# Optimization experiments

Hardware: AMD Instinct MI355X
Metric: run time of the kernel (lower is better)

Reference implementation:

```python
import jax, jax.numpy as jnp
import numpy as np

N, S, D, H = 2048, 16, 128, 8
EPS = 1e-5  # torch.nn.LayerNorm default eps


def setup_inputs() -> dict:
    key = jax.random.key(0)
    ks = jax.random.split(key, 3)
    return {
        "x": jax.random.normal(ks[0], (N, S, D), jnp.float32),
        "Wi": jax.random.normal(ks[1], (H, S, D, D), jnp.float32),
        "Wj": jax.random.normal(ks[2], (H, S, 2 * D, D), jnp.float32),
        "ln1_w": jnp.ones((S, D), jnp.float32),
        "ln1_b": jnp.zeros((S, D), jnp.float32),
        "prelu1_a": jnp.float32(0.25),  # torch PReLU default single param
        "ln2_w": jnp.ones((H, D), jnp.float32),
        "ln2_b": jnp.zeros((H, D), jnp.float32),
        "prelu2_a": jnp.float32(0.25),
    }


def _layernorm2(x, w, b):
    # LayerNorm over the last two dims (matches torch LayerNorm([A, B]))
    mu = jnp.mean(x, axis=(-2, -1), keepdims=True)
    var = jnp.var(x, axis=(-2, -1), keepdims=True)
    return (x - mu) * jax.lax.rsqrt(var + EPS) * w + b


def _prelu(x, a):
    return jnp.where(x >= 0, x, a * x)


def reference(x, Wi, Wj, ln1_w, ln1_b, prelu1_a, ln2_w, ln2_b, prelu2_a):
    n, s, d = x.shape
    h = Wi.shape[0]
    # sort descending along source dim
    idx = jnp.argsort(-x, axis=1)                      # [N,S,D] int
    x_sort = jnp.take_along_axis(x, idx, axis=1)       # [N,S,D]
    # pad with a zero row, take adjacent differences
    pad = jnp.concatenate([x_sort, jnp.zeros((n, 1, d), x.dtype)], axis=1)
    diff = pad[:, :-1, :] - pad[:, 1:, :]              # [N,S,D]
    # positional encoding: cumsum of 2^rank / 2^S
    enc = jnp.cumsum(jnp.exp2(idx.astype(x.dtype)), axis=1) / jnp.asarray(2.0 ** s, x.dtype)
    # per-head, per-source batched matmul with Wi
    se = jnp.einsum('bsd,hsdo->bhso', enc, Wi)         # [N,H,S,D]
    se = _prelu(_layernorm2(se, ln1_w, ln1_b), prelu1_a)  # Dropout in eval mode = identity
    cat = jnp.concatenate(
        [jnp.broadcast_to(diff[:, None, :, :], (n, h, s, d)), se], axis=-1
    )                                                  # [N,H,S,2D]
    out = jnp.einsum('bhsd,hsdo->bho', cat, Wj)        # [N,H,D]
    return _prelu(_layernorm2(out, ln2_w, ln2_b), prelu2_a)
```

## Files before the change

### kernel.cpp

```cpp
#include <hip/hip_runtime.h>

#define N_ 2048
#define S_ 16
#define D_ 128
#define H_ 8
#define EPS_ 1e-5f

typedef unsigned short ushortT;
typedef unsigned int uint32;
typedef __attribute__((ext_vector_type(8))) short short8;
typedef __attribute__((ext_vector_type(8))) unsigned short ushort8;
typedef __attribute__((ext_vector_type(4))) float f32x4;
typedef __attribute__((ext_vector_type(4))) unsigned int uint4v;
typedef __attribute__((ext_vector_type(8))) float float8;

__device__ __forceinline__ ushortT f2bf(float f) {
  union { float f; uint32 u; } c; c.f = f;
  uint32 u = c.u;
  u = (u + 0x7FFFu + ((u >> 16) & 1u)) >> 16;
  return (ushortT)u;
}
__device__ __forceinline__ float bf2f(ushortT b) {
  union { uint32 u; float f; } c; c.u = ((uint32)b) << 16;
  return c.f;
}

__global__ __launch_bounds__(256) void k_prep(const float* __restrict__ x,
                                              ushortT* __restrict__ enc,
                                              ushortT* __restrict__ diff) {
  int g = blockIdx.x * 256 + threadIdx.x;
  int n = g >> 7, d = g & 127;
  const float* xp = x + (size_t)n * (S_ * D_) + d;
  float v[S_];
#pragma unroll
  for (int s = 0; s < S_; ++s) v[s] = xp[s * D_];
  int r[S_];
#pragma unroll
  for (int i = 0; i < S_; ++i) {
    int ri = 0;
#pragma unroll
    for (int j = 0; j < S_; ++j)
      ri += ((v[j] > v[i]) || (v[j] == v[i] && j < i)) ? 1 : 0;
    r[i] = ri;
  }
  float xs[S_ + 1];
#pragma unroll
  for (int s = 0; s < S_; ++s) {
    float acc = 0.f;
#pragma unroll
    for (int i = 0; i < S_; ++i) acc += (r[i] == s) ? v[i] : 0.f;
    xs[s] = acc;
  }
  xs[S_] = 0.f;
  ushortT* ep = enc + (size_t)n * (S_ * D_) + d;
  ushortT* dp = diff + (size_t)n * (S_ * D_) + d;
#pragma unroll
  for (int s = 0; s < S_; ++s) {
    uint32 mm = 0;
#pragma unroll
    for (int i = 0; i < S_; ++i) mm |= (r[i] <= s) ? (1u << i) : 0u;
    ep[s * D_] = f2bf((float)mm * (1.f / 65536.f));
    dp[s * D_] = f2bf(xs[s] - xs[s + 1]);
  }
}

__global__ __launch_bounds__(256) void k_castW(const float* __restrict__ Wi,
                                               const float* __restrict__ Wj,
                                               ushortT* __restrict__ Wit,
                                               ushortT* __restrict__ Wjt) {
  __shared__ ushortT tile[128 * 136];
  int bx = blockIdx.x;
  int t = threadIdx.x;
  if (bx < 128) {
    int hs = bx;
    const float* src = Wi + (size_t)hs * D_ * D_;
#pragma unroll 4
    for (int i = 0; i < 64; ++i) {
      int e = t + 256 * i;
      int dd = e >> 7, o = e & 127;
      tile[dd * 136 + o] = f2bf(src[e]);
    }
    __syncthreads();
    int o = t >> 1, dbase = (t & 1) * 64;
    ushortT* dst = Wit + ((size_t)hs * D_ + o) * D_ + dbase;
#pragma unroll
    for (int c = 0; c < 8; ++c) {
      uint4v pk;
#pragma unroll
      for (int q = 0; q < 4; ++q) {
        ushortT lo = tile[(dbase + c * 8 + q * 2) * 136 + o];
        ushortT hi = tile[(dbase + c * 8 + q * 2 + 1) * 136 + o];
        pk[q] = (uint32)lo | ((uint32)hi << 16);
      }
      *(uint4v*)(dst + c * 8) = pk;
    }
  } else {
    int hs = bx - 128; int h = hs >> 4, s = hs & 15;
    const float* src = Wj + (size_t)hs * 256 * D_;
    for (int half = 0; half < 2; ++half) {
      if (half) __syncthreads();
#pragma unroll 4
      for (int i = 0; i < 64; ++i) {
        int e = t + 256 * i;
        int dd = e >> 7, o = e & 127;
        tile[dd * 136 + o] = f2bf(src[half * 16384 + e]);
      }
      __syncthreads();
      int o = t >> 1, db = (t & 1) * 64;
      ushortT* dst = Wjt + ((size_t)(h * D_ + o)) * (S_ * 256) + s * 256 + half * 128 + db;
#pragma unroll
      for (int c = 0; c < 8; ++c) {
        uint4v pk;
#pragma unroll
        for (int q = 0; q < 4; ++q) {
          ushortT lo = tile[(db + c * 8 + q * 2) * 136 + o];
          ushortT hi = tile[(db + c * 8 + q * 2 + 1) * 136 + o];
          pk[q] = (uint32)lo | ((uint32)hi << 16);
        }
        *(uint4v*)(dst + c * 8) = pk;
      }
    }
  }
}

__global__ __launch_bounds__(256) void k_gemm1(const ushortT* __restrict__ enc,
                                               const ushortT* __restrict__ Wit,
                                               ushortT* __restrict__ se,
                                               float* __restrict__ ssum,
                                               float* __restrict__ ssq) {
  int bt = blockIdx.x, s = blockIdx.y, hp = blockIdx.z;
  int h0 = hp * 4;
  __shared__ ushortT As[128 * 128];
  __shared__ ushortT Bs[128 * 128];
  int tid = threadIdx.x;
  int c16 = tid & 15, prow = tid >> 4;
  int wave = tid >> 6, lane = tid & 63;
  int l15 = lane & 15, lg = lane >> 4;

  ushort8 rb[8];
#pragma unroll
  for (int i = 0; i < 8; ++i) {
    int row = prow + 16 * i;
    int sw = ((c16 ^ (row & 7)) * 8);
    ushort8 va = *(const ushort8*)(enc + (size_t)(bt * 128 + row) * (S_ * D_) + s * D_ + c16 * 8);
    *(ushort8*)(As + row * 128 + sw) = va;
    rb[i] = *(const ushort8*)(Wit + ((size_t)((h0 * S_ + s) * D_) + row) * D_ + c16 * 8);
  }
  __syncthreads();
  short8 afr[4][2];
#pragma unroll
  for (int kk = 0; kk < 4; ++kk)
#pragma unroll
    for (int i = 0; i < 2; ++i) {
      int row = wave * 32 + i * 16 + l15;
      int cc = kk * 4 + lg;
      afr[kk][i] = *(const short8*)(As + row * 128 + ((cc ^ (row & 7)) * 8));
    }

  for (int hh = 0; hh < 4; ++hh) {
    int h = h0 + hh;
    if (hh) __syncthreads();
#pragma unroll
    for (int i = 0; i < 8; ++i) {
      int row = prow + 16 * i;
      *(ushort8*)(Bs + row * 128 + ((c16 ^ (row & 7)) * 8)) = rb[i];
    }
    if (hh < 3) {
#pragma unroll
      for (int i = 0; i < 8; ++i) {
        int row = prow + 16 * i;
        rb[i] = *(const ushort8*)(Wit + ((size_t)(((h + 1) * S_ + s) * D_) + row) * D_ + c16 * 8);
      }
    }
    __syncthreads();
    f32x4 acc[2][8];
#pragma unroll
    for (int i = 0; i < 2; ++i)
#pragma unroll
      for (int j = 0; j < 8; ++j) acc[i][j] = (f32x4)(0.f);
#pragma unroll
    for (int kk = 0; kk < 4; ++kk) {
      int cc = kk * 4 + lg;
      short8 b[8];
#pragma unroll
      for (int j = 0; j < 8; ++j) {
        int row = j * 16 + l15;
        b[j] = *(const short8*)(Bs + row * 128 + ((cc ^ (row & 7)) * 8));
      }
#pragma unroll
      for (int i = 0; i < 2; ++i)
#pragma unroll
        for (int j = 0; j < 8; ++j)
          acc[i][j] = __builtin_amdgcn_mfma_f32_16x16x32_bf16(afr[kk][i], b[j], acc[i][j], 0, 0, 0);
    }
#pragma unroll
    for (int i = 0; i < 2; ++i)
#pragma unroll
      for (int rr = 0; rr < 4; ++rr) {
        int rloc = wave * 32 + i * 16 + lg * 4 + rr;
        int b_g = bt * 128 + rloc;
        float rs = 0.f, rq = 0.f;
#pragma unroll
        for (int j = 0; j < 8; ++j) {
          float val = acc[i][j][rr];
          rs += val; rq += val * val;
        }
#pragma unroll
        for (int m = 1; m <= 8; m <<= 1) {
          rs += __shfl_xor(rs, m);
          rq += __shfl_xor(rq, m);
        }
        if (l15 == 0) {
          ssum[((size_t)s * N_ + b_g) * H_ + h] = rs;
          ssq[((size_t)s * N_ + b_g) * H_ + h] = rq;
        }
      }
    __syncthreads();
#pragma unroll
    for (int i = 0; i < 2; ++i)
#pragma unroll
      for (int rr = 0; rr < 4; ++rr) {
        int row = wave * 32 + i * 16 + lg * 4 + rr;
        int sw = (row & 7) << 3;
#pragma unroll
        for (int j = 0; j < 8; ++j) {
          int o = j * 16 + l15;
          Bs[row * 128 + (o ^ sw)] = f2bf(acc[i][j][rr]);
        }
      }
    __syncthreads();
#pragma unroll
    for (int p = 0; p < 2; ++p) {
      int row = p * 64 + (tid >> 2);
      int sw = (row & 7) << 3;
      int b_g = bt * 128 + row;
      ushortT* dst = se + (((size_t)b_g * H_ + h) * S_ + s) * D_;
#pragma unroll
      for (int q = 0; q < 4; ++q) {
        int o0 = (q * 4 + (tid & 3)) * 8;
        *(uint4v*)(dst + o0) = *(const uint4v*)(Bs + row * 128 + (o0 ^ sw));
      }
    }
  }
}

__global__ __launch_bounds__(256) void k_finalize(const float* __restrict__ ssum,
                                                  const float* __restrict__ ssq,
                                                  float* __restrict__ mr) {
  int t = blockIdx.x * 256 + threadIdx.x;
  float s1 = 0.f, s2 = 0.f;
#pragma unroll
  for (int s = 0; s < S_; ++s) {
    s1 += ssum[(size_t)s * (N_ * H_) + t];
    s2 += ssq[(size_t)s * (N_ * H_) + t];
  }
  float mu = s1 * (1.f / 2048.f);
  float var = s2 * (1.f / 2048.f) - mu * mu;
  mr[t * 2] = mu;
  mr[t * 2 + 1] = rsqrtf(var + EPS_);
}

__global__ __launch_bounds__(256, 3) void k_gemm2(const ushortT* __restrict__ diff,
                                                  const ushortT* __restrict__ se,
                                                  const ushortT* __restrict__ Wjt,
                                                  const float* __restrict__ mr,
                                                  const float* __restrict__ ln1w,
                                                  const float* __restrict__ ln1b,
                                                  const float* __restrict__ pa1,
                                                  float* __restrict__ outp,
                                                  int scount) {
  int bt = blockIdx.x, sh = blockIdx.y, h = blockIdx.z;
  int s0 = sh * scount;
  __shared__ ushortT As[128 * 64];
  __shared__ ushortT Bs[128 * 64];
  int tid = threadIdx.x;
  int c8 = tid & 7, trow = tid >> 3;
  int swst = ((c8 ^ (trow & 7)) * 8);
  int wave = tid >> 6, lane = tid & 63;
  int l15 = lane & 15, lg = lane >> 4;
  int wm = wave >> 1, wn = wave & 1;
  float a1 = pa1[0];

  float mu_r[4], rs_r[4];
  uint32 aoff_d[4], aoff_s[4], boff[4];
#pragma unroll
  for (int i = 0; i < 4; ++i) {
    int row = i * 32 + trow;
    int b_g = bt * 128 + row;
    mu_r[i] = mr[((size_t)b_g * H_ + h) * 2];
    rs_r[i] = mr[((size_t)b_g * H_ + h) * 2 + 1];
    aoff_d[i] = (uint32)b_g * (S_ * D_) + c8 * 8;
    aoff_s[i] = ((uint32)b_g * H_ + h) * (S_ * D_) + c8 * 8;
    boff[i] = (uint32)(h * D_ + row) * (S_ * 256) + c8 * 8;
  }
  ushort8 ra[4], rb[4];
  int nc = scount * 4;
  {
    uint32 add = s0 * D_;
#pragma unroll
    for (int i = 0; i < 4; ++i) {
      ra[i] = *(const ushort8*)(diff + aoff_d[i] + add);
      rb[i] = *(const ushort8*)(Wjt + boff[i] + s0 * 256);
    }
  }
  f32x4 acc[4][4];
#pragma unroll
  for (int i = 0; i < 4; ++i)
#pragma unroll
    for (int j = 0; j < 4; ++j) acc[i][j] = (f32x4)(0.f);

  for (int c = 0; c < nc; ++c) {
    int p = c & 3, s = s0 + (c >> 2);
    if (c) __syncthreads();
    if (p >= 2) {
      float8 w8 = *(const float8*)(ln1w + s * D_ + (p & 1) * 64 + c8 * 8);
      float8 b8 = *(const float8*)(ln1b + s * D_ + (p & 1) * 64 + c8 * 8);
#pragma unroll
      for (int i = 0; i < 4; ++i) {
        ushort8 v = ra[i];
#pragma unroll
        for (int e = 0; e < 8; ++e) {
          float f = bf2f(v[e]);
          float y = (f - mu_r[i]) * rs_r[i] * w8[e] + b8[e];
          y = (y >= 0.f) ? y : a1 * y;
          v[e] = f2bf(y);
        }
        ra[i] = v;
      }
    }
#pragma unroll
    for (int i = 0; i < 4; ++i) {
      int row = i * 32 + trow;
      *(ushort8*)(As + row * 64 + swst) = ra[i];
      *(ushort8*)(Bs + row * 64 + swst) = rb[i];
    }
    if (c + 1 < nc) {
      int cn = c + 1;
      int sn = s0 + (cn >> 2), pn = cn & 3;
      uint32 add = sn * D_ + (pn & 1) * 64;
      uint32 badd = sn * 256 + pn * 64;
#pragma unroll
      for (int i = 0; i < 4; ++i) {
        ra[i] = (pn < 2) ? *(const ushort8*)(diff + aoff_d[i] + add)
                         : *(const ushort8*)(se + aoff_s[i] + add);
        rb[i] = *(const ushort8*)(Wjt + boff[i] + badd);
      }
    }
    __syncthreads();
#pragma unroll
    for (int kk = 0; kk < 2; ++kk) {
      int cc = kk * 4 + lg;
      short8 a[4], b[4];
#pragma unroll
      for (int i = 0; i < 4; ++i) {
        int row = wm * 64 + i * 16 + l15;
        a[i] = *(const short8*)(As + row * 64 + ((cc ^ (row & 7)) * 8));
      }
#pragma unroll
      for (int j = 0; j < 4; ++j) {
        int row = wn * 64 + j * 16 + l15;
        b[j] = *(const short8*)(Bs + row * 64 + ((cc ^ (row & 7)) * 8));
      }
#pragma unroll
      for (int i = 0; i < 4; ++i)
#pragma unroll
        for (int j = 0; j < 4; ++j)
          acc[i][j] = __builtin_amdgcn_mfma_f32_16x16x32_bf16(a[i], b[j], acc[i][j], 0, 0, 0);
    }
  }
#pragma unroll
  for (int i = 0; i < 4; ++i)
#pragma unroll
    for (int j = 0; j < 4; ++j)
#pragma unroll
      for (int rr = 0; rr < 4; ++rr) {
        int b_g = bt * 128 + wm * 64 + i * 16 + lg * 4 + rr;
        int o = wn * 64 + j * 16 + l15;
        outp[(((size_t)sh * N_ + b_g) * H_ + h) * D_ + o] = acc[i][j][rr];
      }
}

__global__ __launch_bounds__(256) void k_ln2(const float* __restrict__ outp,
                                             const float* __restrict__ ln2w,
                                             const float* __restrict__ ln2b,
                                             const float* __restrict__ pa2,
                                             float* __restrict__ out,
                                             int nsplit) {
  int b = blockIdx.x, t = threadIdx.x;
  __shared__ float red[8];
  __shared__ float stats[2];
  f32x4 v = (f32x4)(0.f);
  for (int p = 0; p < nsplit; ++p)
    v += *((const f32x4*)(outp + (size_t)p * (N_ * 1024) + (size_t)b * 1024) + t);
  float s1 = v[0] + v[1] + v[2] + v[3];
  float s2 = v[0] * v[0] + v[1] * v[1] + v[2] * v[2] + v[3] * v[3];
#pragma unroll
  for (int m = 1; m <= 32; m <<= 1) {
    s1 += __shfl_xor(s1, m);
    s2 += __shfl_xor(s2, m);
  }
  int wave = t >> 6, lane = t & 63;
  if (lane == 0) { red[wave] = s1; red[4 + wave] = s2; }
  __syncthreads();
  if (t == 0) {
    float S = red[0] + red[1] + red[2] + red[3];
    float Q = red[4] + red[5] + red[6] + red[7];
    float mu = S * (1.f / 1024.f);
    float var = Q * (1.f / 1024.f) - mu * mu;
    stats[0] = mu; stats[1] = rsqrtf(var + EPS_);
  }
  __syncthreads();
  float mu = stats[0], rstd = stats[1];
  float a2 = pa2[0];
  f32x4 wv = *((const f32x4*)ln2w + t);
  f32x4 bv = *((const f32x4*)ln2b + t);
  f32x4 r;
#pragma unroll
  for (int e = 0; e < 4; ++e) {
    float y = (v[e] - mu) * rstd * wv[e] + bv[e];
    r[e] = (y >= 0.f) ? y : a2 * y;
  }
  *((f32x4*)(out + (size_t)b * 1024) + t) = r;
}

extern "C" void kernel_launch(void* const* d_in, const int* in_sizes, int n_in,
                              void* d_out, int out_size, void* d_ws, size_t ws_size,
                              hipStream_t stream) {
  const float* x    = (const float*)d_in[0];
  const float* Wi   = (const float*)d_in[1];
  const float* Wj   = (const float*)d_in[2];
  const float* ln1w = (const float*)d_in[3];
  const float* ln1b = (const float*)d_in[4];
  const float* pa1  = (const float*)d_in[5];
  const float* ln2w = (const float*)d_in[6];
  const float* ln2b = (const float*)d_in[7];
  const float* pa2  = (const float*)d_in[8];
  char* ws = (char*)d_ws;
  ushortT* se   = (ushortT*)(ws + 0);
  ushortT* diff = (ushortT*)(ws + 67108864);
  ushortT* Wjt  = (ushortT*)(ws + 75497472);
  float*   outp = (float*)(ws + 83886080);
  ushortT* enc  = (ushortT*)(ws + 83886080);
  ushortT* Wit  = (ushortT*)(ws + 92274688);
  float*   ssum = (float*)(ws + 96468992);
  float*   ssq  = (float*)(ws + 97517568);
  float*   out  = (float*)d_out;

  int nsplit = (ws_size >= 117571584ull) ? 4 : 2;
  int scount = S_ / nsplit;
  float* mr = (float*)(ws + 83886080 + (size_t)nsplit * 8388608);

  hipLaunchKernelGGL(k_prep, dim3(1024), dim3(256), 0, stream, x, enc, diff);
  hipLaunchKernelGGL(k_castW, dim3(256), dim3(256), 0, stream, Wi, Wj, Wit, Wjt);
  hipLaunchKernelGGL(k_gemm1, dim3(16, 16, 2), dim3(256), 0, stream, enc, Wit, se, ssum, ssq);
  hipLaunchKernelGGL(k_finalize, dim3(64), dim3(256), 0, stream, ssum, ssq, mr);
  hipLaunchKernelGGL(k_gemm2, dim3(16, nsplit, 8), dim3(256), 0, stream, diff, se, Wjt, mr,
                     ln1w, ln1b, pa1, outp, scount);
  hipLaunchKernelGGL(k_ln2, dim3(2048), dim3(256), 0, stream, outp, ln2w, ln2b, pa2, out, nsplit);
}
```

Baseline: 208.1 us.

## Pre-swizzle gemm2 operands and stream them to LDS with double buffering

k_prep and k_castW now write diff and Wj in a tile-contiguous, pre-swizzled layout. k_gemm2 can then copy 128x64 tiles straight from global memory into LDS with global_load_lds, using double-buffered A/B tiles so loads overlap the MFMA work. The LayerNorm1+PReLU applied to the se half is folded into fused multiply-adds using a precomputed rstd and -mu*rstd, and it packs to bf16 with v_cvt_pk_bf16_f32. Occupancy drops from 3 to 2 blocks per CU because LDS use doubles, and the indexing in the producer kernels gets more involved.

```diff
diff --git a/kernel.cpp b/kernel.cpp
--- a/kernel.cpp
+++ b/kernel.cpp
@@ -27,7 +27,7 @@
 
 __global__ __launch_bounds__(256) void k_prep(const float* __restrict__ x,
                                               ushortT* __restrict__ enc,
-                                              ushortT* __restrict__ diff) {
+                                              ushortT* __restrict__ diff_sw) {
   int g = blockIdx.x * 256 + threadIdx.x;
   int n = g >> 7, d = g & 127;
   const float* xp = x + (size_t)n * (S_ * D_) + d;
@@ -53,21 +53,23 @@
   }
   xs[S_] = 0.f;
   ushortT* ep = enc + (size_t)n * (S_ * D_) + d;
-  ushortT* dp = diff + (size_t)n * (S_ * D_) + d;
+  int btq = n >> 7, rr = n & 127, pp = d >> 6, c8p = (d >> 3) & 7, ee = d & 7;
+  int q = rr * 8 + (c8p ^ (rr & 7));
 #pragma unroll
   for (int s = 0; s < S_; ++s) {
     uint32 mm = 0;
 #pragma unroll
     for (int i = 0; i < S_; ++i) mm |= (r[i] <= s) ? (1u << i) : 0u;
     ep[s * D_] = f2bf((float)mm * (1.f / 65536.f));
-    dp[s * D_] = f2bf(xs[s] - xs[s + 1]);
+    size_t idx = ((((size_t)(btq * 16 + s) * 2 + pp) * 1024) + q) * 8 + ee;
+    diff_sw[idx] = f2bf(xs[s] - xs[s + 1]);
   }
 }
 
 __global__ __launch_bounds__(256) void k_castW(const float* __restrict__ Wi,
                                                const float* __restrict__ Wj,
                                                ushortT* __restrict__ Wit,
-                                               ushortT* __restrict__ Wjt) {
+                                               ushortT* __restrict__ Wjt_sw) {
   __shared__ ushortT tile[128 * 136];
   int bx = blockIdx.x;
   int t = threadIdx.x;
@@ -107,7 +109,8 @@
       }
       __syncthreads();
       int o = t >> 1, db = (t & 1) * 64;
-      ushortT* dst = Wjt + ((size_t)(h * D_ + o)) * (S_ * 256) + s * 256 + half * 128 + db;
+      int part = half * 2 + (t & 1);
+      ushortT* dst = Wjt_sw + ((size_t)(h * 16 + s) * 4 + part) * 8192;
 #pragma unroll
       for (int c = 0; c < 8; ++c) {
         uint4v pk;
@@ -117,7 +120,7 @@
           ushortT hi = tile[(db + c * 8 + q * 2 + 1) * 136 + o];
           pk[q] = (uint32)lo | ((uint32)hi << 16);
         }
-        *(uint4v*)(dst + c * 8) = pk;
+        *(uint4v*)(dst + (o * 8 + (c ^ (o & 7))) * 8) = pk;
       }
     }
   }
@@ -256,13 +259,25 @@
   }
   float mu = s1 * (1.f / 2048.f);
   float var = s2 * (1.f / 2048.f) - mu * mu;
-  mr[t * 2] = mu;
-  mr[t * 2 + 1] = rsqrtf(var + EPS_);
-}
-
-__global__ __launch_bounds__(256, 3) void k_gemm2(const ushortT* __restrict__ diff,
+  float rstd = rsqrtf(var + EPS_);
+  mr[t * 2] = rstd;
+  mr[t * 2 + 1] = -mu * rstd;
+}
+
+#define GLDS_TILE(DST, SRC) do {                                              \
+    const ushortT* sp_ = (SRC) + wave * 512 + lane * 8;                       \
+    ushortT* dp_ = (DST) + wave * 512;                                        \
+    _Pragma("unroll")                                                         \
+    for (int i_ = 0; i_ < 4; ++i_)                                            \
+      __builtin_amdgcn_global_load_lds(                                       \
+          (const __attribute__((address_space(1))) void*)(sp_ + i_ * 2048),   \
+          (__attribute__((address_space(3))) void*)(dp_ + i_ * 2048),         \
+          16, 0, 0);                                                          \
+  } while (0)
+
+__global__ __launch_bounds__(256, 2) void k_gemm2(const ushortT* __restrict__ diff_sw,
                                                   const ushortT* __restrict__ se,
-                                                  const ushortT* __restrict__ Wjt,
+                                                  const ushortT* __restrict__ Wjt_sw,
                                                   const float* __restrict__ mr,
                                                   const float* __restrict__ ln1w,
                                                   const float* __restrict__ ln1b,
@@ -271,103 +286,112 @@
                                                   int scount) {
   int bt = blockIdx.x, sh = blockIdx.y, h = blockIdx.z;
   int s0 = sh * scount;
-  __shared__ ushortT As[128 * 64];
-  __shared__ ushortT Bs[128 * 64];
+  __shared__ ushortT As[2][128 * 64];
+  __shared__ ushortT Bs[2][128 * 64];
   int tid = threadIdx.x;
+  int wave = tid >> 6, lane = tid & 63;
   int c8 = tid & 7, trow = tid >> 3;
   int swst = ((c8 ^ (trow & 7)) * 8);
-  int wave = tid >> 6, lane = tid & 63;
   int l15 = lane & 15, lg = lane >> 4;
   int wm = wave >> 1, wn = wave & 1;
   float a1 = pa1[0];
 
-  float mu_r[4], rs_r[4];
-  uint32 aoff_d[4], aoff_s[4], boff[4];
+  float rs_r[4], nm_r[4];
+  uint32 aoff_s[4];
 #pragma unroll
   for (int i = 0; i < 4; ++i) {
     int row = i * 32 + trow;
     int b_g = bt * 128 + row;
-    mu_r[i] = mr[((size_t)b_g * H_ + h) * 2];
-    rs_r[i] = mr[((size_t)b_g * H_ + h) * 2 + 1];
-    aoff_d[i] = (uint32)b_g * (S_ * D_) + c8 * 8;
+    rs_r[i] = mr[((size_t)b_g * H_ + h) * 2];
+    nm_r[i] = mr[((size_t)b_g * H_ + h) * 2 + 1];
     aoff_s[i] = ((uint32)b_g * H_ + h) * (S_ * D_) + c8 * 8;
-    boff[i] = (uint32)(h * D_ + row) * (S_ * 256) + c8 * 8;
-  }
-  ushort8 ra[4], rb[4];
-  int nc = scount * 4;
-  {
-    uint32 add = s0 * D_;
-#pragma unroll
-    for (int i = 0; i < 4; ++i) {
-      ra[i] = *(const ushort8*)(diff + aoff_d[i] + add);
-      rb[i] = *(const ushort8*)(Wjt + boff[i] + s0 * 256);
-    }
-  }
+  }
+  ushort8 raL[4], raH[4];
   f32x4 acc[4][4];
 #pragma unroll
   for (int i = 0; i < 4; ++i)
 #pragma unroll
     for (int j = 0; j < 4; ++j) acc[i][j] = (f32x4)(0.f);
 
-  for (int c = 0; c < nc; ++c) {
-    int p = c & 3, s = s0 + (c >> 2);
-    if (c) __syncthreads();
-    if (p >= 2) {
-      float8 w8 = *(const float8*)(ln1w + s * D_ + (p & 1) * 64 + c8 * 8);
-      float8 b8 = *(const float8*)(ln1b + s * D_ + (p & 1) * 64 + c8 * 8);
-#pragma unroll
-      for (int i = 0; i < 4; ++i) {
-        ushort8 v = ra[i];
-#pragma unroll
-        for (int e = 0; e < 8; ++e) {
-          float f = bf2f(v[e]);
-          float y = (f - mu_r[i]) * rs_r[i] * w8[e] + b8[e];
-          y = (y >= 0.f) ? y : a1 * y;
-          v[e] = f2bf(y);
-        }
-        ra[i] = v;
-      }
-    }
-#pragma unroll
-    for (int i = 0; i < 4; ++i) {
-      int row = i * 32 + trow;
-      *(ushort8*)(As + row * 64 + swst) = ra[i];
-      *(ushort8*)(Bs + row * 64 + swst) = rb[i];
-    }
-    if (c + 1 < nc) {
-      int cn = c + 1;
-      int sn = s0 + (cn >> 2), pn = cn & 3;
-      uint32 add = sn * D_ + (pn & 1) * 64;
-      uint32 badd = sn * 256 + pn * 64;
-#pragma unroll
-      for (int i = 0; i < 4; ++i) {
-        ra[i] = (pn < 2) ? *(const ushort8*)(diff + aoff_d[i] + add)
-                         : *(const ushort8*)(se + aoff_s[i] + add);
-        rb[i] = *(const ushort8*)(Wjt + boff[i] + badd);
-      }
-    }
-    __syncthreads();
-#pragma unroll
-    for (int kk = 0; kk < 2; ++kk) {
-      int cc = kk * 4 + lg;
-      short8 a[4], b[4];
-#pragma unroll
-      for (int i = 0; i < 4; ++i) {
-        int row = wm * 64 + i * 16 + l15;
-        a[i] = *(const short8*)(As + row * 64 + ((cc ^ (row & 7)) * 8));
-      }
-#pragma unroll
-      for (int j = 0; j < 4; ++j) {
-        int row = wn * 64 + j * 16 + l15;
-        b[j] = *(const short8*)(Bs + row * 64 + ((cc ^ (row & 7)) * 8));
-      }
-#pragma unroll
-      for (int i = 0; i < 4; ++i)
-#pragma unroll
-        for (int j = 0; j < 4; ++j)
-          acc[i][j] = __builtin_amdgcn_mfma_f32_16x16x32_bf16(a[i], b[j], acc[i][j], 0, 0, 0);
-    }
-  }
+#define COMPUTE(XBUF) do {                                                    \
+    _Pragma("unroll")                                                         \
+    for (int kk = 0; kk < 2; ++kk) {                                          \
+      int cc = kk * 4 + lg;                                                   \
+      short8 a[4], b[4];                                                      \
+      _Pragma("unroll")                                                       \
+      for (int i = 0; i < 4; ++i) {                                           \
+        int row = wm * 64 + i * 16 + l15;                                     \
+        a[i] = *(const short8*)(As[XBUF] + row * 64 + ((cc ^ (row & 7)) * 8));\
+      }                                                                       \
+      _Pragma("unroll")                                                       \
+      for (int j = 0; j < 4; ++j) {                                           \
+        int row = wn * 64 + j * 16 + l15;                                     \
+        b[j] = *(const short8*)(Bs[XBUF] + row * 64 + ((cc ^ (row & 7)) * 8));\
+      }                                                                       \
+      _Pragma("unroll")                                                       \
+      for (int i = 0; i < 4; ++i)                                             \
+        _Pragma("unroll")                                                     \
+        for (int j = 0; j < 4; ++j)                                           \
+          acc[i][j] = __builtin_amdgcn_mfma_f32_16x16x32_bf16(a[i], b[j],     \
+                                                              acc[i][j], 0, 0, 0); \
+    } } while (0)
+
+#define TRANSFORM_WRITE(RA, NXBUF, SS, HALF) do {                             \
+    float8 w8 = *(const float8*)(ln1w + (SS) * D_ + (HALF) * 64 + c8 * 8);    \
+    float8 b8 = *(const float8*)(ln1b + (SS) * D_ + (HALF) * 64 + c8 * 8);    \
+    _Pragma("unroll")                                                         \
+    for (int i = 0; i < 4; ++i) {                                             \
+      int row = i * 32 + trow;                                                \
+      float y[8];                                                             \
+      _Pragma("unroll")                                                       \
+      for (int e = 0; e < 8; ++e) {                                           \
+        float f = bf2f((ushortT)RA[i][e]);                                    \
+        float tt = fmaf(f, rs_r[i], nm_r[i]);                                 \
+        float vv = fmaf(tt, w8[e], b8[e]);                                    \
+        y[e] = fmaf(a1, fminf(vv, 0.f), fmaxf(vv, 0.f));                      \
+      }                                                                       \
+      uint4v pk;                                                              \
+      _Pragma("unroll")                                                       \
+      for (int q = 0; q < 4; ++q) {                                           \
+        uint32 rpk;                                                           \
+        asm("v_cvt_pk_bf16_f32 %0, %1, %2" : "=v"(rpk)                        \
+            : "v"(y[2 * q]), "v"(y[2 * q + 1]));                              \
+        pk[q] = rpk;                                                          \
+      }                                                                       \
+      *(uint4v*)(As[NXBUF] + row * 64 + swst) = pk;                           \
+    } } while (0)
+
+  GLDS_TILE(As[0], diff_sw + ((size_t)(bt * 16 + s0) * 2 + 0) * 8192);
+  GLDS_TILE(Bs[0], Wjt_sw + ((size_t)(h * 16 + s0) * 4 + 0) * 8192);
+  __syncthreads();
+
+  for (int si = 0; si < scount; ++si) {
+    int s = s0 + si;
+    int sn = (s + 1 < S_) ? s + 1 : 0;
+#pragma unroll
+    for (int i = 0; i < 4; ++i)
+      raL[i] = *(const ushort8*)(se + aoff_s[i] + s * D_);
+    GLDS_TILE(As[1], diff_sw + ((size_t)(bt * 16 + s) * 2 + 1) * 8192);
+    GLDS_TILE(Bs[1], Wjt_sw + ((size_t)(h * 16 + s) * 4 + 1) * 8192);
+    COMPUTE(0);
+    __syncthreads();
+#pragma unroll
+    for (int i = 0; i < 4; ++i)
+      raH[i] = *(const ushort8*)(se + aoff_s[i] + s * D_ + 64);
+    TRANSFORM_WRITE(raL, 0, s, 0);
+    GLDS_TILE(Bs[0], Wjt_sw + ((size_t)(h * 16 + s) * 4 + 2) * 8192);
+    COMPUTE(1);
+    __syncthreads();
+    TRANSFORM_WRITE(raH, 1, s, 1);
+    GLDS_TILE(Bs[1], Wjt_sw + ((size_t)(h * 16 + s) * 4 + 3) * 8192);
+    COMPUTE(0);
+    __syncthreads();
+    GLDS_TILE(As[0], diff_sw + ((size_t)(bt * 16 + sn) * 2 + 0) * 8192);
+    GLDS_TILE(Bs[0], Wjt_sw + ((size_t)(h * 16 + sn) * 4 + 0) * 8192);
+    COMPUTE(1);
+    __syncthreads();
+  }
+
 #pragma unroll
   for (int i = 0; i < 4; ++i)
 #pragma unroll
@@ -436,25 +460,25 @@
   const float* ln2b = (const float*)d_in[7];
   const float* pa2  = (const float*)d_in[8];
   char* ws = (char*)d_ws;
-  ushortT* se   = (ushortT*)(ws + 0);
-  ushortT* diff = (ushortT*)(ws + 67108864);
-  ushortT* Wjt  = (ushortT*)(ws + 75497472);
-  float*   outp = (float*)(ws + 83886080);
-  ushortT* enc  = (ushortT*)(ws + 83886080);
-  ushortT* Wit  = (ushortT*)(ws + 92274688);
-  float*   ssum = (float*)(ws + 96468992);
-  float*   ssq  = (float*)(ws + 97517568);
-  float*   out  = (float*)d_out;
+  ushortT* se      = (ushortT*)(ws + 0);
+  ushortT* diff_sw = (ushortT*)(ws + 67108864);
+  ushortT* Wjt_sw  = (ushortT*)(ws + 75497472);
+  float*   outp    = (float*)(ws + 83886080);
+  ushortT* enc     = (ushortT*)(ws + 83886080);
+  ushortT* Wit     = (ushortT*)(ws + 92274688);
+  float*   ssum    = (float*)(ws + 96468992);
+  float*   ssq     = (float*)(ws + 97517568);
+  float*   out     = (float*)d_out;
 
   int nsplit = (ws_size >= 117571584ull) ? 4 : 2;
   int scount = S_ / nsplit;
   float* mr = (float*)(ws + 83886080 + (size_t)nsplit * 8388608);
 
-  hipLaunchKernelGGL(k_prep, dim3(1024), dim3(256), 0, stream, x, enc, diff);
-  hipLaunchKernelGGL(k_castW, dim3(256), dim3(256), 0, stream, Wi, Wj, Wit, Wjt);
+  hipLaunchKernelGGL(k_prep, dim3(1024), dim3(256), 0, stream, x, enc, diff_sw);
+  hipLaunchKernelGGL(k_castW, dim3(256), dim3(256), 0, stream, Wi, Wj, Wit, Wjt_sw);
   hipLaunchKernelGGL(k_gemm1, dim3(16, 16, 2), dim3(256), 0, stream, enc, Wit, se, ssum, ssq);
   hipLaunchKernelGGL(k_finalize, dim3(64), dim3(256), 0, stream, ssum, ssq, mr);
-  hipLaunchKernelGGL(k_gemm2, dim3(16, nsplit, 8), dim3(256), 0, stream, diff, se, Wjt, mr,
+  hipLaunchKernelGGL(k_gemm2, dim3(16, nsplit, 8), dim3(256), 0, stream, diff_sw, se, Wjt_sw, mr,
                      ln1w, ln1b, pa1, outp, scount);
   hipLaunchKernelGGL(k_ln2, dim3(2048), dim3(256), 0, stream, outp, ln2w, ln2b, pa2, out, nsplit);
 }
```

Measured after the change: 196.1 us. 5.8% less time.
